# Optimization experiments

Measured on AMD Instinct MI355X. Metric: run time of the kernel, lower is better.

Reference implementation:

```python
import jax, jax.numpy as jnp
import numpy as np
from jax import lax

SIZE = 28  # canvas size (init kwarg)


def setup_inputs() -> dict:
    key = jax.random.key(0)
    k_xy, k_i = jax.random.split(key)
    B, T = 1024, 64
    # per-step (x, y) coordinates in [-0.5, 0.5] (matches range grid), intensity in [0, 1]
    xy = jax.random.uniform(k_xy, (B, T, 2), dtype=jnp.float32, minval=-0.5, maxval=0.5)
    inten = jax.random.uniform(k_i, (B, T, 1), dtype=jnp.float32)
    x = jnp.concatenate([xy, inten], axis=-1)  # (B, T, 3)
    return {"x": x}


def reference(x) -> jnp.ndarray:
    # x: (B, T, 3) strokes; mode='position', return_sequences=False
    B = x.shape[0]
    rng = (jnp.arange(SIZE, dtype=x.dtype) / SIZE - 0.5)  # (SIZE,)
    g = (SIZE / 2.0) ** 2  # (1/sigma)^2 with sigma = 2/SIZE

    def step(image, inp):
        # inp: (B, 3)
        px = jnp.exp(-jnp.square(rng[None, :] - inp[:, 0:1]) * g)  # (B, SIZE)
        py = jnp.exp(-jnp.square(rng[None, :] - inp[:, 1:2]) * g)  # (B, SIZE)
        stroke = inp[:, 2][:, None, None] * py[:, :, None] * px[:, None, :]  # (B, SIZE, SIZE)
        image = jnp.minimum(jnp.maximum(image, stroke), 1.0)
        return image, None

    image0 = jnp.zeros((B, SIZE, SIZE), dtype=x.dtype)
    image, _ = lax.scan(step, image0, jnp.swapaxes(x, 0, 1))  # scan over T
    return image[..., None]  # (B, SIZE, SIZE, 1)
```

## Files before the change

kernel.cpp:

```cpp
#include <hip/hip_runtime.h>

#define CANVAS 28
#define TSTEPS 64
#define GCONST 196.0f

__global__ __launch_bounds__(256) void draw_image_kernel(
    const float* __restrict__ x,
    float* __restrict__ out)
{
    const int b   = blockIdx.x;
    const int tid = threadIdx.x;

    __shared__ float4 s_abc[TSTEPS];

    if (tid < TSTEPS) {
        const float xv = x[b * (TSTEPS * 3) + tid * 3 + 0];
        const float yv = x[b * (TSTEPS * 3) + tid * 3 + 1];
        const float iv = x[b * (TSTEPS * 3) + tid * 3 + 2];
        const float li = __logf(iv);
        s_abc[tid] = make_float4(li - GCONST * (xv * xv + yv * yv),
                                 2.0f * GCONST * xv,
                                 2.0f * GCONST * yv, 0.0f);
    }
    __syncthreads();

    if (tid < 196) {
        const int row = tid / 7;
        const int cg  = tid - row * 7;
        const float ri = (float)row * (1.0f / CANVAS) - 0.5f;
        float rj[4];
        #pragma unroll
        for (int k = 0; k < 4; ++k)
            rj[k] = (float)(cg * 4 + k) * (1.0f / CANVAS) - 0.5f;

        float m0 = -1e30f, m1 = -1e30f, m2 = -1e30f, m3 = -1e30f;

        #pragma unroll 8
        for (int t = 0; t < TSTEPS; ++t) {
            const float4 abc = s_abc[t];
            const float h = __builtin_fmaf(abc.z, ri, abc.x);
            m0 = fmaxf(m0, __builtin_fmaf(abc.y, rj[0], h));
            m1 = fmaxf(m1, __builtin_fmaf(abc.y, rj[1], h));
            m2 = fmaxf(m2, __builtin_fmaf(abc.y, rj[2], h));
            m3 = fmaxf(m3, __builtin_fmaf(abc.y, rj[3], h));
        }

        const float pc = -GCONST * ri * ri;
        float4 o;
        o.x = fminf(__expf(m0 + __builtin_fmaf(-GCONST, rj[0] * rj[0], pc)), 1.0f);
        o.y = fminf(__expf(m1 + __builtin_fmaf(-GCONST, rj[1] * rj[1], pc)), 1.0f);
        o.z = fminf(__expf(m2 + __builtin_fmaf(-GCONST, rj[2] * rj[2], pc)), 1.0f);
        o.w = fminf(__expf(m3 + __builtin_fmaf(-GCONST, rj[3] * rj[3], pc)), 1.0f);

        float* outp = out + b * (CANVAS * CANVAS) + row * CANVAS + cg * 4;
        *reinterpret_cast<float4*>(outp) = o;
    }
}

extern "C" void kernel_launch(void* const* d_in, const int* in_sizes, int n_in,
                              void* d_out, int out_size, void* d_ws, size_t ws_size,
                              hipStream_t stream) {
    const float* x = (const float*)d_in[0];
    float* out = (float*)d_out;
    const int B = in_sizes[0] / (TSTEPS * 3);
    draw_image_kernel<<<dim3(B), dim3(256), 0, stream>>>(x, out);
}
```

Before: 11.66 us.

## Broadcast per-step stroke params via readlane instead of shared memory and barrier

New measurement: 11.22 us. 3.8% less time.

```diff
diff --git a/kernel.cpp b/kernel.cpp
--- a/kernel.cpp
+++ b/kernel.cpp
@@ -4,56 +4,59 @@
 #define TSTEPS 64
 #define GCONST 196.0f
 
-__global__ __launch_bounds__(256) void draw_image_kernel(
+__global__ __launch_bounds__(128) void draw_image_kernel(
     const float* __restrict__ x,
     float* __restrict__ out)
 {
-    const int b   = blockIdx.x;
-    const int tid = threadIdx.x;
+    const int b    = blockIdx.x;
+    const int tid  = threadIdx.x;
+    const int wave = tid >> 6;
+    const int lane = tid & 63;
 
-    __shared__ float4 s_abc[TSTEPS];
+    const float xv = x[b * 192 + lane * 3 + 0];
+    const float yv = x[b * 192 + lane * 3 + 1];
+    const float iv = x[b * 192 + lane * 3 + 2];
+    const float vA  = __logf(iv) - GCONST * (xv * xv + yv * yv);
+    const float vCx = 2.0f * GCONST * xv;
+    const float vCy = 2.0f * GCONST * yv;
 
-    if (tid < TSTEPS) {
-        const float xv = x[b * (TSTEPS * 3) + tid * 3 + 0];
-        const float yv = x[b * (TSTEPS * 3) + tid * 3 + 1];
-        const float iv = x[b * (TSTEPS * 3) + tid * 3 + 2];
-        const float li = __logf(iv);
-        s_abc[tid] = make_float4(li - GCONST * (xv * xv + yv * yv),
-                                 2.0f * GCONST * xv,
-                                 2.0f * GCONST * yv, 0.0f);
+    const int lrow = lane >> 2;
+    const int lcg  = lane & 3;
+    const bool active = (lrow < 14);
+    const int row = 14 * wave + (active ? lrow : 0);
+    const float ri = (float)row * (1.0f / CANVAS) - 0.5f;
+
+    float rj[7];
+    #pragma unroll
+    for (int k = 0; k < 7; ++k)
+        rj[k] = (float)(lcg * 7 + k) * (1.0f / CANVAS) - 0.5f;
+
+    float m[7];
+    #pragma unroll
+    for (int k = 0; k < 7; ++k) m[k] = -1e30f;
+
+    #pragma unroll
+    for (int t = 0; t < TSTEPS; ++t) {
+        const float A  = __builtin_bit_cast(float,
+            __builtin_amdgcn_readlane(__builtin_bit_cast(int, vA),  t));
+        const float cx = __builtin_bit_cast(float,
+            __builtin_amdgcn_readlane(__builtin_bit_cast(int, vCx), t));
+        const float cy = __builtin_bit_cast(float,
+            __builtin_amdgcn_readlane(__builtin_bit_cast(int, vCy), t));
+        const float h = __builtin_fmaf(cy, ri, A);
+        #pragma unroll
+        for (int k = 0; k < 7; ++k)
+            m[k] = fmaxf(m[k], __builtin_fmaf(cx, rj[k], h));
     }
-    __syncthreads();
 
-    if (tid < 196) {
-        const int row = tid / 7;
-        const int cg  = tid - row * 7;
-        const float ri = (float)row * (1.0f / CANVAS) - 0.5f;
-        float rj[4];
+    if (active) {
+        const float pc = -GCONST * ri * ri;
+        float* outp = out + b * (CANVAS * CANVAS) + row * CANVAS + lcg * 7;
         #pragma unroll
-        for (int k = 0; k < 4; ++k)
-            rj[k] = (float)(cg * 4 + k) * (1.0f / CANVAS) - 0.5f;
-
-        float m0 = -1e30f, m1 = -1e30f, m2 = -1e30f, m3 = -1e30f;
-
-        #pragma unroll 8
-        for (int t = 0; t < TSTEPS; ++t) {
-            const float4 abc = s_abc[t];
-            const float h = __builtin_fmaf(abc.z, ri, abc.x);
-            m0 = fmaxf(m0, __builtin_fmaf(abc.y, rj[0], h));
-            m1 = fmaxf(m1, __builtin_fmaf(abc.y, rj[1], h));
-            m2 = fmaxf(m2, __builtin_fmaf(abc.y, rj[2], h));
-            m3 = fmaxf(m3, __builtin_fmaf(abc.y, rj[3], h));
+        for (int k = 0; k < 7; ++k) {
+            const float p = __builtin_fmaf(-GCONST, rj[k] * rj[k], pc);
+            outp[k] = fminf(__expf(m[k] + p), 1.0f);
         }
-
-        const float pc = -GCONST * ri * ri;
-        float4 o;
-        o.x = fminf(__expf(m0 + __builtin_fmaf(-GCONST, rj[0] * rj[0], pc)), 1.0f);
-        o.y = fminf(__expf(m1 + __builtin_fmaf(-GCONST, rj[1] * rj[1], pc)), 1.0f);
-        o.z = fminf(__expf(m2 + __builtin_fmaf(-GCONST, rj[2] * rj[2], pc)), 1.0f);
-        o.w = fminf(__expf(m3 + __builtin_fmaf(-GCONST, rj[3] * rj[3], pc)), 1.0f);
-
-        float* outp = out + b * (CANVAS * CANVAS) + row * CANVAS + cg * 4;
-        *reinterpret_cast<float4*>(outp) = o;
     }
 }
 
@@ -63,5 +66,5 @@
     const float* x = (const float*)d_in[0];
     float* out = (float*)d_out;
     const int B = in_sizes[0] / (TSTEPS * 3);
-    draw_image_kernel<<<dim3(B), dim3(256), 0, stream>>>(x, out);
+    draw_image_kernel<<<dim3(B), dim3(128), 0, stream>>>(x, out);
 }
```
